# Performance work log

Hardware: AMD Instinct MI355X
Metric: run time of the kernel (lower is better)

The kernel has to match this reference:

```python
import jax, jax.numpy as jnp
import numpy as np

VOCAB = 65
N_EMBED = 384
BLOCK = 256
N_HEAD = 6
HEAD_SIZE = 4  # forward uses sa_heads = MultiHeadAttention(4), NOT the Block stack
B, T = 128, 256


def setup_inputs() -> dict:
    key = jax.random.key(0)
    ks = jax.random.split(key, 16)
    s = lambda *sh: 0.02
    inp = {
        "idx": jax.random.randint(ks[0], (B, T), 0, VOCAB),
        "targets": jax.random.randint(ks[1], (B, T), 0, VOCAB),
        "tok_emb": jax.random.normal(ks[2], (VOCAB, N_EMBED), jnp.float32) * 0.02,
        "pos_emb": jax.random.normal(ks[3], (BLOCK, N_EMBED), jnp.float32) * 0.02,
        "Wq": jax.random.normal(ks[4], (N_HEAD, N_EMBED, HEAD_SIZE), jnp.float32) * 0.05,
        "Wk": jax.random.normal(ks[5], (N_HEAD, N_EMBED, HEAD_SIZE), jnp.float32) * 0.05,
        "Wv": jax.random.normal(ks[6], (N_HEAD, N_EMBED, HEAD_SIZE), jnp.float32) * 0.05,
        "Wproj": jax.random.normal(ks[7], (N_HEAD * HEAD_SIZE, N_EMBED), jnp.float32) * 0.05,
        "bproj": jnp.zeros((N_EMBED,), jnp.float32),
        "W1": jax.random.normal(ks[8], (N_EMBED, 4 * N_EMBED), jnp.float32) * 0.02,
        "b1": jnp.zeros((4 * N_EMBED,), jnp.float32),
        "W2": jax.random.normal(ks[9], (4 * N_EMBED, N_EMBED), jnp.float32) * 0.02,
        "b2": jnp.zeros((N_EMBED,), jnp.float32),
        "Wlm": jax.random.normal(ks[10], (N_EMBED, VOCAB), jnp.float32) * 0.02,
        "blm": jnp.zeros((VOCAB,), jnp.float32),
    }
    return inp


def _forward(idx, targets, tok_emb, pos_emb, Wq, Wk, Wv, Wproj, bproj, W1, b1, W2, b2, Wlm, blm):
    Bb, Tt = idx.shape
    x = tok_emb[idx] + pos_emb[:Tt]  # [B,T,C]
    # multi-head attention (manual, causal). NOTE: source scales by n_embed**-0.5 (C of input), not head_size.
    q = jnp.einsum("btc,hcd->bhtd", x, Wq)
    k = jnp.einsum("btc,hcd->bhtd", x, Wk)
    v = jnp.einsum("btc,hcd->bhtd", x, Wv)
    scores = jnp.einsum("bhtd,bhsd->bhts", q, k) * (N_EMBED ** -0.5)
    causal = jnp.tril(jnp.ones((Tt, Tt), bool))
    scores = jnp.where(causal, scores, -jnp.inf)
    w = jax.nn.softmax(scores, axis=-1)  # dropout = identity in eval
    attn = jnp.einsum("bhts,bhsd->bhtd", w, v)
    attn = attn.transpose(0, 2, 1, 3).reshape(Bb, Tt, N_HEAD * HEAD_SIZE)
    x = attn @ Wproj + bproj
    # feed-forward
    x = jax.nn.relu(x @ W1 + b1) @ W2 + b2
    logits = x @ Wlm + blm  # [B,T,V]
    logits_flat = logits.reshape(Bb * Tt, VOCAB)
    t_flat = targets.reshape(Bb * Tt)
    logp = jax.nn.log_softmax(logits_flat, axis=-1)
    loss = -jnp.mean(jnp.take_along_axis(logp, t_flat[:, None], axis=1))
    return logits_flat, loss


def reference(idx, targets, tok_emb, pos_emb, Wq, Wk, Wv, Wproj, bproj, W1, b1, W2, b2, Wlm, blm):
    return _forward(idx, targets, tok_emb, pos_emb, Wq, Wk, Wv, Wproj, bproj, W1, b1, W2, b2, Wlm, blm)
```

## Files before the change

kernel.cpp:

```cpp
#include <hip/hip_runtime.h>
#include <hip/hip_bf16.h>
#include <math.h>

typedef __hip_bfloat16 bf16;
typedef __attribute__((ext_vector_type(8))) short bf16x8;
typedef __attribute__((ext_vector_type(4))) float f32x4;
typedef __attribute__((ext_vector_type(8))) int i32x8;
typedef __attribute__((ext_vector_type(4))) int i32x4;
typedef unsigned char u8;
typedef unsigned int u32;

#define T_SEQ   256
#define C_EMB   384
#define NH      6
#define HS      4
#define NB      128
#define NTOK    (NB * T_SEQ)
#define VOC     65
#define FFDIM   1536
#define QKVW    72
#define PROJK   32
#define XROWS   (VOC * T_SEQ)

#define X2_SCALE    128.0f
#define W1_SCALE    128.0f
#define FF1_DESCALE (1.0f / (128.0f * 128.0f))
#define H1_SCALE    512.0f
#define W2_SCALE    128.0f
#define FF2_DESCALE (1.0f / (512.0f * 128.0f))

__device__ __forceinline__ float bf2f(bf16 x) { return __bfloat162float(x); }
__device__ __forceinline__ bf16  f2b(float x) { return __float2bfloat16(x); }
__device__ __forceinline__ short f2s(float x) { bf16 b = __float2bfloat16(x); return *reinterpret_cast<short*>(&b); }
__device__ __forceinline__ u8 f2fp8(float x) {
    return (u8)(__builtin_amdgcn_cvt_pk_fp8_f32(x, x, 0, false) & 0xff);
}
__device__ __forceinline__ u32 pk4fp8(const float* w) {
    int p = __builtin_amdgcn_cvt_pk_fp8_f32(w[0], w[1], 0, false);
    p = __builtin_amdgcn_cvt_pk_fp8_f32(w[2], w[3], p, true);
    return (u32)p;
}

__device__ __forceinline__ void glds16(const void* g, void* l) {
    __builtin_amdgcn_global_load_lds((const __attribute__((address_space(1))) void*)g,
                                     (__attribute__((address_space(3))) void*)l, 16, 0, 0);
}

__global__ void pack_all_kernel(const float* __restrict__ Wq, const float* __restrict__ Wk,
                                const float* __restrict__ Wv, const float* __restrict__ Wlm,
                                const float* __restrict__ Wproj,
                                const float* __restrict__ W1, const float* __restrict__ W2,
                                const float* __restrict__ tok_emb, const float* __restrict__ pos_emb,
                                bf16* __restrict__ WqkvT, bf16* __restrict__ WlmT,
                                bf16* __restrict__ WprojT, u8* __restrict__ W1P,
                                u8* __restrict__ W2P, bf16* __restrict__ xtab,
                                float* __restrict__ lossbuf) {
    int blk = blockIdx.x;
    int t = threadIdx.x;
    if (blk == 0 && t == 0) { lossbuf[0] = 0.f; ((int*)lossbuf)[1] = 0; }
    if (blk < 128) {
        int n = blk;
        for (int c = t; c < C_EMB; c += 256) {
            float v = 0.f;
            if (n < QKVW) {
                int sel = n / 24, r = n % 24, h = r >> 2, d = r & 3;
                const float* W = (sel == 0) ? Wq : (sel == 1) ? Wk : Wv;
                v = W[(h * C_EMB + c) * HS + d];
            }
            WqkvT[(size_t)n * C_EMB + c] = f2b(v);
        }
    } else if (blk < 256) {
        int n = blk - 128;
        for (int c = t; c < C_EMB; c += 256)
            WlmT[(size_t)n * C_EMB + c] = f2b(n < VOC ? Wlm[(size_t)c * VOC + n] : 0.f);
    } else if (blk < 640) {
        int n = blk - 256;
        int k = t;
        if (k < PROJK)
            WprojT[(size_t)n * PROJK + k] = f2b(k < 24 ? Wproj[(size_t)k * C_EMB + n] : 0.f);
    } else if (blk < 640 + 288) {
        int fb = blk - 640;
        int n16 = fb / 3, kk = fb % 3;
        int b0 = t * 8;
        int l = b0 >> 5;
        int j0 = b0 & 31;
        int n = n16 * 16 + (l & 15);
        int kb = kk * 128 + (l >> 4) * 32 + j0;
        union { u8 b[8]; uint2 u; } pk;
        #pragma unroll
        for (int e = 0; e < 8; ++e)
            pk.b[e] = f2fp8(W1[(size_t)(kb + e) * FFDIM + n] * W1_SCALE);
        *(uint2*)&W1P[(size_t)fb * 2048 + b0] = pk.u;
    } else if (blk < 640 + 576) {
        int fb = blk - 640 - 288;
        int n16 = fb / 12, kc = fb % 12;
        int b0 = t * 8;
        int l = b0 >> 5;
        int j0 = b0 & 31;
        int n = n16 * 16 + (l & 15);
        int kb = kc * 128 + (l >> 4) * 32 + j0;
        union { u8 b[8]; uint2 u; } pk;
        #pragma unroll
        for (int e = 0; e < 8; ++e)
            pk.b[e] = f2fp8(W2[(size_t)(kb + e) * C_EMB + n] * W2_SCALE);
        *(uint2*)&W2P[(size_t)fb * 2048 + b0] = pk.u;
    } else {
        int base = (blk - (640 + 576)) * 4;
        for (int r = 0; r < 4; ++r) {
            int row = base + r;
            int id = row >> 8, tt = row & 255;
            const float* te = tok_emb + (size_t)id * C_EMB;
            const float* pe = pos_emb + (size_t)tt * C_EMB;
            bf16* dst = xtab + (size_t)row * C_EMB;
            for (int c = t; c < C_EMB; c += 256)
                dst[c] = f2b(te[c] + pe[c]);
        }
    }
}

__global__ __launch_bounds__(512)
void qkv_gather_kernel(const int* __restrict__ idx, const bf16* __restrict__ xtab,
                       const bf16* __restrict__ Bt, float* __restrict__ outf) {
    __shared__ __align__(16) u8 As[16384];
    __shared__ __align__(16) u8 Bs[16384];
    __shared__ int rowid[128];
    int tid = threadIdx.x, lane = tid & 63, wave = tid >> 6;
    int bm = blockIdx.x * 128;
    int wm = (wave & 1) * 64, wn = (wave >> 1) * 32;
    int lrow = lane & 15, kq = lane >> 4;
    if (tid < 128) { int token = bm + tid; rowid[tid] = idx[token] * T_SEQ + (token & (T_SEQ - 1)); }
    __syncthreads();

    int r0 = tid >> 3;
    int s0 = (((tid & 7) * 16) - (r0 & 7) * 16) & 127;
    int c1 = tid + 512;
    int r1 = c1 >> 3;
    int s1 = (((c1 & 7) * 16) - (r1 & 7) * 16) & 127;
    const u8* xb = (const u8*)xtab;
    const u8* bb = (const u8*)Bt;
    long gA0 = (long)rowid[r0] * 768 + s0;
    long gA1 = (long)rowid[r1] * 768 + s1;
    long gB0 = (long)r0 * 768 + s0;
    long gB1 = (long)r1 * 768 + s1;
    int ro = (lrow & 7) * 16;

    f32x4 acc[4][2] = {};
    for (int k0 = 0; k0 < 768; k0 += 128) {
        glds16(xb + gA0 + k0, As + (size_t)tid * 16);
        glds16(xb + gA1 + k0, As + (size_t)c1 * 16);
        glds16(bb + gB0 + k0, Bs + (size_t)tid * 16);
        glds16(bb + gB1 + k0, Bs + (size_t)c1 * 16);
        __syncthreads();
        #pragma unroll
        for (int ks = 0; ks < 2; ++ks) {
            int off = (ks * 64 + kq * 16 + ro) & 127;
            bf16x8 af[4], bff[2];
            #pragma unroll
            for (int i = 0; i < 4; ++i)
                af[i] = *(const bf16x8*)&As[(size_t)(wm + i * 16 + lrow) * 128 + off];
            #pragma unroll
            for (int i = 0; i < 2; ++i)
                bff[i] = *(const bf16x8*)&Bs[(size_t)(wn + i * 16 + lrow) * 128 + off];
            #pragma unroll
            for (int mi = 0; mi < 4; ++mi)
                #pragma unroll
                for (int ni = 0; ni < 2; ++ni)
                    acc[mi][ni] = __builtin_amdgcn_mfma_f32_16x16x32_bf16(af[mi], bff[ni], acc[mi][ni], 0, 0, 0);
        }
        __syncthreads();
    }

    #pragma unroll
    for (int ni = 0; ni < 2; ++ni) {
        int col = wn + ni * 16 + lrow;
        if (col >= QKVW) continue;
        #pragma unroll
        for (int mi = 0; mi < 4; ++mi) {
            int orow = bm + wm + mi * 16 + kq * 4;
            #pragma unroll
            for (int r = 0; r < 4; ++r)
                outf[(size_t)(orow + r) * QKVW + col] = acc[mi][ni][r];
        }
    }
}

__global__ void attn_kernel(const float* __restrict__ qkv,
                            bf16* __restrict__ attnT) {
    int bh = blockIdx.x;
    int b = bh / NH, h = bh % NH;
    int t = threadIdx.x;
    __shared__ float4 kv[T_SEQ][2];
    const float* base = qkv + (size_t)(b * T_SEQ) * QKVW;
    kv[t][0] = *(const float4*)(base + t * QKVW + 24 + h * HS);
    kv[t][1] = *(const float4*)(base + t * QKVW + 48 + h * HS);
    __syncthreads();
    const float scale = 0.05103103630798288f;
    float4 q = *(const float4*)(base + t * QKVW + h * HS);
    float qx = q.x * scale, qy = q.y * scale, qz = q.z * scale, qw = q.w * scale;
    float sum0 = 0.f, sum1 = 0.f;
    float o0x = 0.f, o0y = 0.f, o0z = 0.f, o0w = 0.f;
    float o1x = 0.f, o1y = 0.f, o1z = 0.f, o1w = 0.f;
    int s = 0;
    for (; s + 1 <= t; s += 2) {
        float4 k0 = kv[s][0],     v0 = kv[s][1];
        float4 k1 = kv[s + 1][0], v1 = kv[s + 1][1];
        float p0 = __expf(qx * k0.x + qy * k0.y + qz * k0.z + qw * k0.w);
        float p1 = __expf(qx * k1.x + qy * k1.y + qz * k1.z + qw * k1.w);
        sum0 += p0; sum1 += p1;
        o0x += p0 * v0.x; o0y += p0 * v0.y; o0z += p0 * v0.z; o0w += p0 * v0.w;
        o1x += p1 * v1.x; o1y += p1 * v1.y; o1z += p1 * v1.z; o1w += p1 * v1.w;
    }
    if (s <= t) {
        float4 k0 = kv[s][0], v0 = kv[s][1];
        float p0 = __expf(qx * k0.x + qy * k0.y + qz * k0.z + qw * k0.w);
        sum0 += p0;
        o0x += p0 * v0.x; o0y += p0 * v0.y; o0z += p0 * v0.z; o0w += p0 * v0.w;
    }
    float inv = 1.f / (sum0 + sum1);
    bf16* out = attnT + (size_t)(b * T_SEQ + t) * PROJK + h * HS;
    out[0] = f2b((o0x + o1x) * inv);
    out[1] = f2b((o0y + o1y) * inv);
    out[2] = f2b((o0z + o1z) * inv);
    out[3] = f2b((o0w + o1w) * inv);
    if (h == 0) {
        bf16* pad = attnT + (size_t)(b * T_SEQ + t) * PROJK + 24;
        *(uint4*)pad = uint4{0, 0, 0, 0};
    }
}

__global__ __launch_bounds__(512, 2)
void ff_mega_kernel(const bf16* __restrict__ attnT, const bf16* __restrict__ WprojT,
                    const float* __restrict__ bproj,
                    const u8* __restrict__ W1P, const float* __restrict__ b1,
                    const u8* __restrict__ W2P, const float* __restrict__ b2,
                    bf16* __restrict__ x3) {
    __shared__ __align__(16) u8 smem[98304];
    u8* x2_lds = smem;
    u8* h1t    = smem + 49152;
    short* As_p = (short*)(smem + 49152);
    short* Bs_p = (short*)(smem + 57344);

    int tid  = threadIdx.x;
    int lane = tid & 63;
    int wave = tid >> 6;
    int bm   = blockIdx.x * 128;
    int lrow  = lane & 15;
    int khalf = lane >> 4;
    int wm  = (wave & 1) * 64;
    int wn6 = (wave >> 1) * 96;
    int wn4 = (wave >> 1) * 64;

    {
        int row = tid >> 2;
        int i0 = (tid & 3) * 16;
        int selem = ((i0 - ((row >> 1) & 3) * 16) & 63) >> 1;
        glds16(attnT + (size_t)(bm + row) * PROJK + selem, As_p + (size_t)tid * 8);
        #pragma unroll
        for (int p = 0; p < 3; ++p) {
            int c = tid + p * 512;
            int rowb = c >> 2;
            int sel2 = (((c & 3) * 16 - ((rowb >> 1) & 3) * 16) & 63) >> 1;
            glds16(WprojT + (size_t)rowb * PROJK + sel2, Bs_p + (size_t)c * 8);
        }
    }
    __syncthreads();

    f32x4 accp[4][6] = {};
    {
        int arot16 = ((lrow >> 1) & 3) * 16;
        int roff = ((khalf * 16 + arot16) & 63) >> 1;
        bf16x8 afp[4], bfp[6];
        #pragma unroll
        for (int i = 0; i < 4; ++i)
            afp[i] = *(const bf16x8*)&As_p[(size_t)(wm + i * 16 + lrow) * 32 + roff];
        #pragma unroll
        for (int i = 0; i < 6; ++i)
            bfp[i] = *(const bf16x8*)&Bs_p[(size_t)(wn6 + i * 16 + lrow) * 32 + roff];
        #pragma unroll
        for (int mi = 0; mi < 4; ++mi)
            #pragma unroll
            for (int ni = 0; ni < 6; ++ni)
                accp[mi][ni] = __builtin_amdgcn_mfma_f32_16x16x32_bf16(bfp[ni], afp[mi], accp[mi][ni], 0, 0, 0);
    }

    #pragma unroll
    for (int mi = 0; mi < 4; ++mi) {
        int m = wm + mi * 16 + lrow;
        #pragma unroll
        for (int ni = 0; ni < 6; ++ni) {
            int n0 = wn6 + ni * 16 + khalf * 4;
            float4 bv = *(const float4*)(bproj + n0);
            float w[4];
            w[0] = (accp[mi][ni][0] + bv.x) * X2_SCALE;
            w[1] = (accp[mi][ni][1] + bv.y) * X2_SCALE;
            w[2] = (accp[mi][ni][2] + bv.z) * X2_SCALE;
            w[3] = (accp[mi][ni][3] + bv.w) * X2_SCALE;
            *(u32*)&x2_lds[(size_t)(n0 >> 7) * 16384 + (size_t)m * 128 +
                           (((n0 & 127) + (m & 7) * 16) & 127)] = pk4fp8(w);
        }
    }
    __syncthreads();

    int arot8 = (lrow & 7) * 16;
    int off0 = (khalf * 32 + arot8) & 127;
    int off1 = (off0 + 16) & 127;

    f32x4 acc1[4][4] = {};
    f32x4 acc2[4][6] = {};

    for (int nt = 0; nt < 6; ++nt) {
        #pragma unroll
        for (int kk = 0; kk < 3; ++kk) {
            const u8* abase = x2_lds + (size_t)kk * 16384;
            i32x8 a[4];
            #pragma unroll
            for (int i = 0; i < 4; ++i) {
                const u8* rp = abase + (size_t)(wm + i * 16 + lrow) * 128;
                i32x4 lo = *(const i32x4*)(rp + off0);
                i32x4 hi = *(const i32x4*)(rp + off1);
                a[i][0]=lo[0]; a[i][1]=lo[1]; a[i][2]=lo[2]; a[i][3]=lo[3];
                a[i][4]=hi[0]; a[i][5]=hi[1]; a[i][6]=hi[2]; a[i][7]=hi[3];
            }
            const u8* wbase = W1P + ((size_t)((nt * 16 + (wave >> 1) * 4) * 3 + kk)) * 2048
                                  + (size_t)lane * 32;
            i32x8 b[4];
            #pragma unroll
            for (int j = 0; j < 4; ++j) {
                const u8* p = wbase + (size_t)j * 3 * 2048;
                i32x4 lo = *(const i32x4*)p;
                i32x4 hi = *(const i32x4*)(p + 16);
                b[j][0]=lo[0]; b[j][1]=lo[1]; b[j][2]=lo[2]; b[j][3]=lo[3];
                b[j][4]=hi[0]; b[j][5]=hi[1]; b[j][6]=hi[2]; b[j][7]=hi[3];
            }
            #pragma unroll
            for (int mi = 0; mi < 4; ++mi)
                #pragma unroll
                for (int j = 0; j < 4; ++j)
                    acc1[mi][j] = __builtin_amdgcn_mfma_scale_f32_16x16x128_f8f6f4(
                        b[j], a[mi], acc1[mi][j], 0, 0,
                        0, 0x7f7f7f7f, 0, 0x7f7f7f7f);
        }

        #pragma unroll
        for (int mi = 0; mi < 4; ++mi) {
            int m = wm + mi * 16 + lrow;
            #pragma unroll
            for (int ni = 0; ni < 4; ++ni) {
                int n0 = wn4 + ni * 16 + khalf * 4;
                float4 bv = *(const float4*)(b1 + nt * 256 + n0);
                float w[4];
                w[0] = fmaxf(acc1[mi][ni][0] * FF1_DESCALE + bv.x, 0.f) * H1_SCALE;
                w[1] = fmaxf(acc1[mi][ni][1] * FF1_DESCALE + bv.y, 0.f) * H1_SCALE;
                w[2] = fmaxf(acc1[mi][ni][2] * FF1_DESCALE + bv.z, 0.f) * H1_SCALE;
                w[3] = fmaxf(acc1[mi][ni][3] * FF1_DESCALE + bv.w, 0.f) * H1_SCALE;
                *(u32*)&h1t[(size_t)m * 256 + ((n0 + (m & 7) * 16) & 255)] = pk4fp8(w);
                acc1[mi][ni] = f32x4{0.f, 0.f, 0.f, 0.f};
            }
        }
        __syncthreads();

        #pragma unroll
        for (int sk = 0; sk < 2; ++sk) {
            i32x8 a2[4];
            #pragma unroll
            for (int i = 0; i < 4; ++i) {
                const u8* rp = h1t + (size_t)(wm + i * 16 + lrow) * 256;
                int o0 = (sk * 128 + khalf * 32 + arot8) & 255;
                int o1 = (sk * 128 + khalf * 32 + 16 + arot8) & 255;
                i32x4 lo = *(const i32x4*)(rp + o0);
                i32x4 hi = *(const i32x4*)(rp + o1);
                a2[i][0]=lo[0]; a2[i][1]=lo[1]; a2[i][2]=lo[2]; a2[i][3]=lo[3];
                a2[i][4]=hi[0]; a2[i][5]=hi[1]; a2[i][6]=hi[2]; a2[i][7]=hi[3];
            }
            int kc = nt * 2 + sk;
            #pragma unroll
            for (int half = 0; half < 2; ++half) {
                i32x8 bw[3];
                #pragma unroll
                for (int j = 0; j < 3; ++j) {
                    int n16 = (wave >> 1) * 6 + half * 3 + j;
                    const u8* p = W2P + ((size_t)n16 * 12 + kc) * 2048 + (size_t)lane * 32;
                    i32x4 lo = *(const i32x4*)p;
                    i32x4 hi = *(const i32x4*)(p + 16);
                    bw[j][0]=lo[0]; bw[j][1]=lo[1]; bw[j][2]=lo[2]; bw[j][3]=lo[3];
                    bw[j][4]=hi[0]; bw[j][5]=hi[1]; bw[j][6]=hi[2]; bw[j][7]=hi[3];
                }
                #pragma unroll
                for (int mi = 0; mi < 4; ++mi)
                    #pragma unroll
                    for (int j = 0; j < 3; ++j)
                        acc2[mi][half * 3 + j] = __builtin_amdgcn_mfma_scale_f32_16x16x128_f8f6f4(
                            bw[j], a2[mi], acc2[mi][half * 3 + j], 0, 0,
                            0, 0x7f7f7f7f, 0, 0x7f7f7f7f);
            }
        }
        __syncthreads();
    }

    u8* Ep = smem;
    #pragma unroll
    for (int mi = 0; mi < 4; ++mi) {
        int m = wm + mi * 16 + lrow;
        #pragma unroll
        for (int ni = 0; ni < 6; ++ni) {
            int n0 = wn6 + ni * 16 + khalf * 4;
            float4 bv = *(const float4*)(b2 + n0);
            union { short s[4]; uint2 u; } pk;
            pk.s[0] = f2s(acc2[mi][ni][0] * FF2_DESCALE + bv.x);
            pk.s[1] = f2s(acc2[mi][ni][1] * FF2_DESCALE + bv.y);
            pk.s[2] = f2s(acc2[mi][ni][2] * FF2_DESCALE + bv.z);
            pk.s[3] = f2s(acc2[mi][ni][3] * FF2_DESCALE + bv.w);
            *(uint2*)&Ep[(size_t)m * 768 + ((n0 >> 7) << 8) +
                         ((((n0 & 127) * 2) + (m & 7) * 16) & 255)] = pk.u;
        }
    }
    __syncthreads();
    #pragma unroll
    for (int p = 0; p < 12; ++p) {
        int c = tid + p * 512;
        int row = c / 48;
        int sl = c - row * 48;
        int g0 = sl * 16;
        int chunk = g0 >> 8;
        int loc = g0 & 255;
        uint4 v = *(const uint4*)&Ep[(size_t)row * 768 + (chunk << 8) +
                                     ((loc + (row & 7) * 16) & 255)];
        *(uint4*)((u8*)x3 + (size_t)(bm + row) * 768 + g0) = v;
    }
}

__global__ __launch_bounds__(512)
void lm_loss_kernel(const bf16* __restrict__ A, const bf16* __restrict__ Bt,
                    const float* __restrict__ bias, const int* __restrict__ targets,
                    float* __restrict__ outf, float* __restrict__ lossbuf,
                    float* __restrict__ out_loss, int M, int K) {
    __shared__ short As[128][32];
    __shared__ short Bs[128][32];
    __shared__ float Ls[128][66];
    __shared__ float red[128];
    int tid  = threadIdx.x;
    int lane = tid & 63;
    int wave = tid >> 6;
    int bm = blockIdx.x * 128;
    int wm = (wave & 1) * 64;
    int wn = (wave >> 1) * 32;
    int lrow  = lane & 15;
    int khalf = lane >> 4;

    int row = tid >> 2;
    int i0 = (tid & 3) * 16;
    int selem = ((i0 - ((row >> 1) & 3) * 16) & 63) >> 1;
    int arot = ((lrow >> 1) & 3) * 16;
    int roff = ((khalf * 16 + arot) & 63) >> 1;

    f32x4 acc[4][2] = {};
    for (int k0 = 0; k0 < K; k0 += 32) {
        glds16(A  + (size_t)(bm + row) * K + k0 + selem, (short*)As + (size_t)tid * 8);
        glds16(Bt + (size_t)row * K + k0 + selem,        (short*)Bs + (size_t)tid * 8);
        __syncthreads();

        bf16x8 af[4], bff[2];
        #pragma unroll
        for (int i = 0; i < 4; ++i)
            af[i] = *(const bf16x8*)&As[wm + i * 16 + lrow][roff];
        #pragma unroll
        for (int i = 0; i < 2; ++i)
            bff[i] = *(const bf16x8*)&Bs[wn + i * 16 + lrow][roff];
        #pragma unroll
        for (int mi = 0; mi < 4; ++mi)
            #pragma unroll
            for (int ni = 0; ni < 2; ++ni)
                acc[mi][ni] = __builtin_amdgcn_mfma_f32_16x16x32_bf16(af[mi], bff[ni], acc[mi][ni], 0, 0, 0);
        __syncthreads();
    }

    #pragma unroll
    for (int ni = 0; ni < 2; ++ni) {
        int col = wn + ni * 16 + lrow;
        if (col >= VOC) continue;
        float bv = bias[col];
        #pragma unroll
        for (int mi = 0; mi < 4; ++mi) {
            int lr = wm + mi * 16 + khalf * 4;
            #pragma unroll
            for (int r = 0; r < 4; ++r) {
                float v = acc[mi][ni][r] + bv;
                outf[(size_t)(bm + lr + r) * VOC + col] = v;
                Ls[lr + r][col] = v;
            }
        }
    }
    __syncthreads();

    if (tid < 128) {
        int token = bm + tid;
        int tgt = targets[token];
        float m = -1e30f, s = 0.f;
        #pragma unroll 8
        for (int c = 0; c < VOC; ++c) {
            float v = Ls[tid][c];
            float mn = fmaxf(m, v);
            s = s * __expf(m - mn) + __expf(v - mn);
            m = mn;
        }
        red[tid] = m + logf(s) - Ls[tid][tgt];
    }
    __syncthreads();
    if (tid < 64) {
        float s = red[tid] + red[tid + 64];
        #pragma unroll
        for (int off = 32; off > 0; off >>= 1) s += __shfl_xor(s, off);
        if (tid == 0) {
            atomicAdd(&lossbuf[0], s);
            __threadfence();
            int done = atomicAdd(&((int*)lossbuf)[1], 1);
            if (done == (NTOK / 128) - 1) {
                __threadfence();
                float total = atomicAdd(&lossbuf[0], 0.0f);
                out_loss[0] = total / (float)NTOK;
            }
        }
    }
}

extern "C" void kernel_launch(void* const* d_in, const int* in_sizes, int n_in,
                              void* d_out, int out_size, void* d_ws, size_t ws_size,
                              hipStream_t stream) {
    const int*   idx     = (const int*)  d_in[0];
    const int*   targets = (const int*)  d_in[1];
    const float* tok_emb = (const float*)d_in[2];
    const float* pos_emb = (const float*)d_in[3];
    const float* Wq      = (const float*)d_in[4];
    const float* Wk      = (const float*)d_in[5];
    const float* Wv      = (const float*)d_in[6];
    const float* Wproj   = (const float*)d_in[7];
    const float* bproj   = (const float*)d_in[8];
    const float* W1      = (const float*)d_in[9];
    const float* b1      = (const float*)d_in[10];
    const float* W2      = (const float*)d_in[11];
    const float* b2      = (const float*)d_in[12];
    const float* Wlm     = (const float*)d_in[13];
    const float* blm     = (const float*)d_in[14];

    char* ws = (char*)d_ws;
    bf16*  WprojT = (bf16*) (ws + 0);
    float* qkvbuf = (float*)(ws + 25165824);
    bf16*  attnT  = (bf16*) (ws + 34603008);
    bf16*  xtab   = (bf16*) (ws + 37748736);
    bf16*  x3     = (bf16*) (ws + 163577856);
    float* lossbuf= (float*)(ws + 188743680);
    u8*    W1P    = (u8*)   (ws + 188874752);
    u8*    W2P    = (u8*)   (ws + 190054400);
    bf16*  WqkvT  = (bf16*) (ws + 191234048);
    bf16*  WlmT   = (bf16*) (ws + 191332352);

    float* out_logits = (float*)d_out;
    float* out_loss   = out_logits + (size_t)NTOK * VOC;

    pack_all_kernel<<<640 + 576 + XROWS / 4, 256, 0, stream>>>(
        Wq, Wk, Wv, Wlm, Wproj, W1, W2, tok_emb, pos_emb,
        WqkvT, WlmT, WprojT, W1P, W2P, xtab, lossbuf);

    qkv_gather_kernel<<<NTOK / 128, 512, 0, stream>>>(idx, xtab, WqkvT, qkvbuf);
    attn_kernel<<<NB * NH, T_SEQ, 0, stream>>>(qkvbuf, attnT);

    ff_mega_kernel<<<NTOK / 128, 512, 0, stream>>>(attnT, WprojT, bproj,
                                                   W1P, b1, W2P, b2, x3);

    lm_loss_kernel<<<NTOK / 128, 512, 0, stream>>>(x3, WlmT, blm, targets,
                                                   out_logits, lossbuf, out_loss, NTOK, C_EMB);
}
```

Baseline: 214.1 us.

## Double ff_mega_kernel waves to 16 with 32-row wave tiles

The fused FF kernel now launches 1024 threads per block instead of 512. The waves are rearranged as a 4x4 grid, so each wave covers 32 rows instead of 64, and its accumulator arrays are halved. Weight fragments are loaded one at a time and consumed right away instead of being buffered as arrays, to lower register pressure. The aim is more waves in flight to hide global weight-load latency. In exchange, each wave reloads the same W1/W2 fragments for fewer rows, which raises weight traffic per MFMA, and the launch bound asks for 4 waves per EU, which may force register spilling.

```diff
diff --git a/kernel.cpp b/kernel.cpp
--- a/kernel.cpp
+++ b/kernel.cpp
@@ -228,7 +228,7 @@
     }
 }
 
-__global__ __launch_bounds__(512, 2)
+__global__ __launch_bounds__(1024, 4)
 void ff_mega_kernel(const bf16* __restrict__ attnT, const bf16* __restrict__ WprojT,
                     const float* __restrict__ bproj,
                     const u8* __restrict__ W1P, const float* __restrict__ b1,
@@ -243,48 +243,54 @@
     int tid  = threadIdx.x;
     int lane = tid & 63;
     int wave = tid >> 6;
+    int wrow = wave & 3;
+    int wcol = wave >> 2;
     int bm   = blockIdx.x * 128;
     int lrow  = lane & 15;
     int khalf = lane >> 4;
-    int wm  = (wave & 1) * 64;
-    int wn6 = (wave >> 1) * 96;
-    int wn4 = (wave >> 1) * 64;
-
-    {
+    int wm  = wrow * 32;
+    int wn6 = wcol * 96;
+    int wn4 = wcol * 64;
+
+    if (tid < 512) {
         int row = tid >> 2;
         int i0 = (tid & 3) * 16;
         int selem = ((i0 - ((row >> 1) & 3) * 16) & 63) >> 1;
         glds16(attnT + (size_t)(bm + row) * PROJK + selem, As_p + (size_t)tid * 8);
-        #pragma unroll
-        for (int p = 0; p < 3; ++p) {
-            int c = tid + p * 512;
-            int rowb = c >> 2;
-            int sel2 = (((c & 3) * 16 - ((rowb >> 1) & 3) * 16) & 63) >> 1;
-            glds16(WprojT + (size_t)rowb * PROJK + sel2, Bs_p + (size_t)c * 8);
-        }
-    }
-    __syncthreads();
-
-    f32x4 accp[4][6] = {};
+    }
+    {
+        int rowb = tid >> 2;
+        int sel2 = (((tid & 3) * 16 - ((rowb >> 1) & 3) * 16) & 63) >> 1;
+        glds16(WprojT + (size_t)rowb * PROJK + sel2, Bs_p + (size_t)tid * 8);
+        int c = tid + 1024;
+        if (c < 1536) {
+            int rb = c >> 2;
+            int s2 = (((c & 3) * 16 - ((rb >> 1) & 3) * 16) & 63) >> 1;
+            glds16(WprojT + (size_t)rb * PROJK + s2, Bs_p + (size_t)c * 8);
+        }
+    }
+    __syncthreads();
+
+    f32x4 accp[2][6] = {};
     {
         int arot16 = ((lrow >> 1) & 3) * 16;
         int roff = ((khalf * 16 + arot16) & 63) >> 1;
-        bf16x8 afp[4], bfp[6];
-        #pragma unroll
-        for (int i = 0; i < 4; ++i)
+        bf16x8 afp[2], bfp[6];
+        #pragma unroll
+        for (int i = 0; i < 2; ++i)
             afp[i] = *(const bf16x8*)&As_p[(size_t)(wm + i * 16 + lrow) * 32 + roff];
         #pragma unroll
         for (int i = 0; i < 6; ++i)
             bfp[i] = *(const bf16x8*)&Bs_p[(size_t)(wn6 + i * 16 + lrow) * 32 + roff];
         #pragma unroll
-        for (int mi = 0; mi < 4; ++mi)
+        for (int mi = 0; mi < 2; ++mi)
             #pragma unroll
             for (int ni = 0; ni < 6; ++ni)
                 accp[mi][ni] = __builtin_amdgcn_mfma_f32_16x16x32_bf16(bfp[ni], afp[mi], accp[mi][ni], 0, 0, 0);
     }
 
     #pragma unroll
-    for (int mi = 0; mi < 4; ++mi) {
+    for (int mi = 0; mi < 2; ++mi) {
         int m = wm + mi * 16 + lrow;
         #pragma unroll
         for (int ni = 0; ni < 6; ++ni) {
@@ -305,44 +311,42 @@
     int off0 = (khalf * 32 + arot8) & 127;
     int off1 = (off0 + 16) & 127;
 
-    f32x4 acc1[4][4] = {};
-    f32x4 acc2[4][6] = {};
+    f32x4 acc1[2][4] = {};
+    f32x4 acc2[2][6] = {};
 
     for (int nt = 0; nt < 6; ++nt) {
         #pragma unroll
         for (int kk = 0; kk < 3; ++kk) {
             const u8* abase = x2_lds + (size_t)kk * 16384;
-            i32x8 a[4];
-            #pragma unroll
-            for (int i = 0; i < 4; ++i) {
+            i32x8 a[2];
+            #pragma unroll
+            for (int i = 0; i < 2; ++i) {
                 const u8* rp = abase + (size_t)(wm + i * 16 + lrow) * 128;
                 i32x4 lo = *(const i32x4*)(rp + off0);
                 i32x4 hi = *(const i32x4*)(rp + off1);
                 a[i][0]=lo[0]; a[i][1]=lo[1]; a[i][2]=lo[2]; a[i][3]=lo[3];
                 a[i][4]=hi[0]; a[i][5]=hi[1]; a[i][6]=hi[2]; a[i][7]=hi[3];
             }
-            const u8* wbase = W1P + ((size_t)((nt * 16 + (wave >> 1) * 4) * 3 + kk)) * 2048
+            const u8* wbase = W1P + ((size_t)((nt * 16 + wcol * 4) * 3 + kk)) * 2048
                                   + (size_t)lane * 32;
-            i32x8 b[4];
             #pragma unroll
             for (int j = 0; j < 4; ++j) {
                 const u8* p = wbase + (size_t)j * 3 * 2048;
                 i32x4 lo = *(const i32x4*)p;
                 i32x4 hi = *(const i32x4*)(p + 16);
-                b[j][0]=lo[0]; b[j][1]=lo[1]; b[j][2]=lo[2]; b[j][3]=lo[3];
-                b[j][4]=hi[0]; b[j][5]=hi[1]; b[j][6]=hi[2]; b[j][7]=hi[3];
-            }
-            #pragma unroll
-            for (int mi = 0; mi < 4; ++mi)
+                i32x8 b;
+                b[0]=lo[0]; b[1]=lo[1]; b[2]=lo[2]; b[3]=lo[3];
+                b[4]=hi[0]; b[5]=hi[1]; b[6]=hi[2]; b[7]=hi[3];
                 #pragma unroll
-                for (int j = 0; j < 4; ++j)
+                for (int mi = 0; mi < 2; ++mi)
                     acc1[mi][j] = __builtin_amdgcn_mfma_scale_f32_16x16x128_f8f6f4(
-                        b[j], a[mi], acc1[mi][j], 0, 0,
+                        b, a[mi], acc1[mi][j], 0, 0,
                         0, 0x7f7f7f7f, 0, 0x7f7f7f7f);
-        }
-
-        #pragma unroll
-        for (int mi = 0; mi < 4; ++mi) {
+            }
+        }
+
+        #pragma unroll
+        for (int mi = 0; mi < 2; ++mi) {
             int m = wm + mi * 16 + lrow;
             #pragma unroll
             for (int ni = 0; ni < 4; ++ni) {
@@ -361,9 +365,9 @@
 
         #pragma unroll
         for (int sk = 0; sk < 2; ++sk) {
-            i32x8 a2[4];
-            #pragma unroll
-            for (int i = 0; i < 4; ++i) {
+            i32x8 a2[2];
+            #pragma unroll
+            for (int i = 0; i < 2; ++i) {
                 const u8* rp = h1t + (size_t)(wm + i * 16 + lrow) * 256;
                 int o0 = (sk * 128 + khalf * 32 + arot8) & 255;
                 int o1 = (sk * 128 + khalf * 32 + 16 + arot8) & 255;
@@ -375,23 +379,21 @@
             int kc = nt * 2 + sk;
             #pragma unroll
             for (int half = 0; half < 2; ++half) {
-                i32x8 bw[3];
                 #pragma unroll
                 for (int j = 0; j < 3; ++j) {
-                    int n16 = (wave >> 1) * 6 + half * 3 + j;
+                    int n16 = wcol * 6 + half * 3 + j;
                     const u8* p = W2P + ((size_t)n16 * 12 + kc) * 2048 + (size_t)lane * 32;
                     i32x4 lo = *(const i32x4*)p;
                     i32x4 hi = *(const i32x4*)(p + 16);
-                    bw[j][0]=lo[0]; bw[j][1]=lo[1]; bw[j][2]=lo[2]; bw[j][3]=lo[3];
-                    bw[j][4]=hi[0]; bw[j][5]=hi[1]; bw[j][6]=hi[2]; bw[j][7]=hi[3];
+                    i32x8 bw;
+                    bw[0]=lo[0]; bw[1]=lo[1]; bw[2]=lo[2]; bw[3]=lo[3];
+                    bw[4]=hi[0]; bw[5]=hi[1]; bw[6]=hi[2]; bw[7]=hi[3];
+                    #pragma unroll
+                    for (int mi = 0; mi < 2; ++mi)
+                        acc2[mi][half * 3 + j] = __builtin_amdgcn_mfma_scale_f32_16x16x128_f8f6f4(
+                            bw, a2[mi], acc2[mi][half * 3 + j], 0, 0,
+                            0, 0x7f7f7f7f, 0, 0x7f7f7f7f);
                 }
-                #pragma unroll
-                for (int mi = 0; mi < 4; ++mi)
-                    #pragma unroll
-                    for (int j = 0; j < 3; ++j)
-                        acc2[mi][half * 3 + j] = __builtin_amdgcn_mfma_scale_f32_16x16x128_f8f6f4(
-                            bw[j], a2[mi], acc2[mi][half * 3 + j], 0, 0,
-                            0, 0x7f7f7f7f, 0, 0x7f7f7f7f);
             }
         }
         __syncthreads();
@@ -399,7 +401,7 @@
 
     u8* Ep = smem;
     #pragma unroll
-    for (int mi = 0; mi < 4; ++mi) {
+    for (int mi = 0; mi < 2; ++mi) {
         int m = wm + mi * 16 + lrow;
         #pragma unroll
         for (int ni = 0; ni < 6; ++ni) {
@@ -416,8 +418,8 @@
     }
     __syncthreads();
     #pragma unroll
-    for (int p = 0; p < 12; ++p) {
-        int c = tid + p * 512;
+    for (int p = 0; p < 6; ++p) {
+        int c = tid + p * 1024;
         int row = c / 48;
         int sl = c - row * 48;
         int g0 = sl * 16;
@@ -564,8 +566,8 @@
     qkv_gather_kernel<<<NTOK / 128, 512, 0, stream>>>(idx, xtab, WqkvT, qkvbuf);
     attn_kernel<<<NB * NH, T_SEQ, 0, stream>>>(qkvbuf, attnT);
 
-    ff_mega_kernel<<<NTOK / 128, 512, 0, stream>>>(attnT, WprojT, bproj,
-                                                   W1P, b1, W2P, b2, x3);
+    ff_mega_kernel<<<NTOK / 128, 1024, 0, stream>>>(attnT, WprojT, bproj,
+                                                    W1P, b1, W2P, b2, x3);
 
     lm_loss_kernel<<<NTOK / 128, 512, 0, stream>>>(x3, WlmT, blm, targets,
                                                    out_logits, lossbuf, out_loss, NTOK, C_EMB);
```

New measurement: 243.2 us. 13.6% more time.
